# Performance work log

Hardware: AMD Instinct MI355X
Metric: run time of the kernel (lower is better)

The kernel has to match this reference:

```python
import jax, jax.numpy as jnp
import numpy as np

N_QUBITS = 8
N_LAYERS = 2
DIM = 1 << N_QUBITS

# Precompute Pauli-Z eigenvalues per qubit (PennyLane: wire 0 = most significant bit)
_idx = np.arange(DIM)
_bits = ((_idx[None, :] >> (N_QUBITS - 1 - np.arange(N_QUBITS)[:, None])) & 1)  # [n, 2^n]
Z_EIG = jnp.asarray(1.0 - 2.0 * _bits, dtype=jnp.float32)                      # [n, 2^n]
# CZ diagonal signs for adjacent pairs (q, q+1)
CZ_SIGN = jnp.asarray(1.0 - 2.0 * (_bits[:-1] * _bits[1:]), dtype=jnp.float32)  # [n-1, 2^n]


def _rx(t):
    c = jnp.cos(0.5 * t).astype(jnp.complex64)
    s = jnp.sin(0.5 * t).astype(jnp.complex64)
    return jnp.stack([jnp.stack([c, -1j * s], -1), jnp.stack([-1j * s, c], -1)], -2)


def _ry(t):
    c = jnp.cos(0.5 * t).astype(jnp.complex64)
    s = jnp.sin(0.5 * t).astype(jnp.complex64)
    return jnp.stack([jnp.stack([c, -s], -1), jnp.stack([s, c], -1)], -2)


def _rz(t):
    e = jnp.exp(-0.5j * t.astype(jnp.complex64))
    z = jnp.zeros_like(e)
    return jnp.stack([jnp.stack([e, z], -1), jnp.stack([z, jnp.conj(e)], -1)], -2)


def _apply_1q(state, gate, q):
    # state: [B, 2^n]; gate: [B,2,2] (data-dependent angle) or [2,2] (shared weight)
    B = state.shape[0]
    L, R = 1 << q, 1 << (N_QUBITS - q - 1)
    st = state.reshape(B, L, 2, R)
    if gate.ndim == 3:
        st = jnp.einsum('bij,bljr->blir', gate, st)
    else:
        st = jnp.einsum('ij,bljr->blir', gate, st)
    return st.reshape(B, DIM)


def _circuit(angles, q_weights):
    # angles: [B, 3*n] real; q_weights: [n_layers, 2*n]
    B = angles.shape[0]
    state = jnp.zeros((B, DIM), dtype=jnp.complex64).at[:, 0].set(1.0)
    for l in range(N_LAYERS):
        for q in range(N_QUBITS):
            state = _apply_1q(state, _rx(angles[:, 3 * q]), q)
            state = _apply_1q(state, _ry(angles[:, 3 * q + 1]), q)
            state = _apply_1q(state, _rz(angles[:, 3 * q + 2]), q)
        for q in range(N_QUBITS):  # ansatz 1: hardware-efficient RY+RZ
            state = _apply_1q(state, _ry(q_weights[l, q]), q)
            state = _apply_1q(state, _rz(q_weights[l, q + N_QUBITS]), q)
        for q in range(N_QUBITS - 1):  # CZ chain (diagonal)
            state = state * CZ_SIGN[q]
    probs = state.real ** 2 + state.imag ** 2          # [B, 2^n]
    return probs @ Z_EIG.T                              # [B, n] expval PauliZ


def setup_inputs() -> dict:
    key = jax.random.key(0)
    ks = jax.random.split(key, 6)
    B = 8192
    return {
        'x': jax.random.normal(ks[0], (B, 64), dtype=jnp.float32),
        'W_adapter': jax.random.normal(ks[1], (3 * N_QUBITS, 64), dtype=jnp.float32) * 0.1,
        'b_adapter': jax.random.normal(ks[2], (3 * N_QUBITS,), dtype=jnp.float32) * 0.1,
        'q_weights': jax.random.normal(ks[3], (N_LAYERS, 2 * N_QUBITS), dtype=jnp.float32),
        'W_fc': jax.random.normal(ks[4], (1, N_QUBITS), dtype=jnp.float32) * 0.1,
        'b_fc': jax.random.normal(ks[5], (1,), dtype=jnp.float32) * 0.1,
    }


def reference(x, W_adapter, b_adapter, q_weights, W_fc, b_fc):
    angles = jnp.arctan(x @ W_adapter.T + b_adapter)   # [B, 3n]
    expvals = _circuit(angles, q_weights)              # [B, n]
    return expvals @ W_fc.T + b_fc                     # [B, 1]
```

## Files before the change

kernel.cpp:

```cpp
#include <hip/hip_runtime.h>
#include <math.h>

#define NQ 8
#define NL 2

template <int CTRL, int RM, int BM>
__device__ __forceinline__ float dpp_add(float v) {
    int o = __builtin_amdgcn_update_dpp(0, __float_as_int(v), CTRL, RM, BM, true);
    return v + __int_as_float(o);
}

__device__ __forceinline__ float wave_total(float v) {
    v = dpp_add<0xB1, 0xF, 0xF>(v);
    v = dpp_add<0x4E, 0xF, 0xF>(v);
    v = dpp_add<0x114, 0xF, 0xE>(v);
    v = dpp_add<0x118, 0xF, 0xC>(v);
    v = dpp_add<0x142, 0xA, 0xF>(v);
    v = dpp_add<0x143, 0xC, 0xF>(v);
    return __int_as_float(__builtin_amdgcn_readlane(__float_as_int(v), 63));
}

__device__ __forceinline__ float read_lane(float v, int l) {
    return __int_as_float(__builtin_amdgcn_readlane(__float_as_int(v), l));
}

template <int P>
__device__ __forceinline__ float partner(float v) {
    int vi = __float_as_int(v);
    if constexpr (P == 0) {
        return __int_as_float(__builtin_amdgcn_update_dpp(vi, vi, 0xB1, 0xF, 0xF, false));
    } else if constexpr (P == 1) {
        return __int_as_float(__builtin_amdgcn_update_dpp(vi, vi, 0x4E, 0xF, 0xF, false));
    } else if constexpr (P == 2) {
        int a = __builtin_amdgcn_update_dpp(vi, vi, 0x104, 0xF, 0x5, false);
        a = __builtin_amdgcn_update_dpp(a, vi, 0x114, 0xF, 0xA, false);
        return __int_as_float(a);
    } else if constexpr (P == 3) {
        int a = __builtin_amdgcn_update_dpp(vi, vi, 0x108, 0xF, 0x3, false);
        a = __builtin_amdgcn_update_dpp(a, vi, 0x118, 0xF, 0xC, false);
        return __int_as_float(a);
    } else if constexpr (P == 4) {
        return __shfl_xor(v, 16, 64);
    } else {
        return __shfl_xor(v, 32, 64);
    }
}

struct SU2 { float ar, ai, br, bi; };

__device__ __forceinline__ void pair_gate(float& r0, float& i0, float& r1, float& i1,
                                          const SU2 g) {
    float nr0 = g.ar * r0 - g.ai * i0 - g.br * r1 - g.bi * i1;
    float ni0 = g.ar * i0 + g.ai * r0 + g.bi * r1 - g.br * i1;
    float nr1 = g.br * r0 - g.bi * i0 + g.ar * r1 + g.ai * i1;
    float ni1 = g.br * i0 + g.bi * r0 + g.ar * i1 - g.ai * r1;
    r0 = nr0; i0 = ni0; r1 = nr1; i1 = ni1;
}

template <int P>
__device__ __forceinline__ void apply_gate(int lane, float (&r)[4], float (&i)[4],
                                           const SU2 g) {
    if constexpr (P == 7) {
        pair_gate(r[0], i[0], r[2], i[2], g);
        pair_gate(r[1], i[1], r[3], i[3], g);
    } else if constexpr (P == 6) {
        pair_gate(r[0], i[0], r[1], i[1], g);
        pair_gate(r[2], i[2], r[3], i[3], g);
    } else {
        float sg = ((lane >> P) & 1) ? 1.0f : -1.0f;
        float Ai = -sg * g.ai;
        float Br =  sg * g.br;
#pragma unroll
        for (int t = 0; t < 4; ++t) {
            float pr = partner<P>(r[t]);
            float pi = partner<P>(i[t]);
            float nr = g.ar * r[t] - Ai * i[t] + Br * pr - g.bi * pi;
            float ni = g.ar * i[t] + Ai * r[t] + Br * pi + g.bi * pr;
            r[t] = nr; i[t] = ni;
        }
    }
}

template <bool LAST>
__device__ __forceinline__ SU2 compose(float ca, float sa, float cb, float sb,
                                       float zc, float zs, float cd, float sd,
                                       float wc, float ws) {
    float pr = cb * ca, pi = sb * sa;
    float qr = sb * ca, qi = -cb * sa;
    float a1r = zc * pr + zs * pi, a1i = zc * pi - zs * pr;
    float b1r = zc * qr - zs * qi, b1i = zc * qi + zs * qr;
    float a2r = cd * a1r - sd * b1r, a2i = cd * a1i - sd * b1i;
    float b2r = sd * a1r + cd * b1r, b2i = sd * a1i + cd * b1i;
    if constexpr (LAST) {
        return {a2r, a2i, b2r, b2i};
    } else {
        float a3r = wc * a2r + ws * a2i, a3i = wc * a2i - ws * a2r;
        float b3r = wc * b2r - ws * b2i, b3i = wc * b2i + ws * b2r;
        return {a3r, a3i, b3r, b3i};
    }
}

template <int L, int Q>
__device__ __forceinline__ void do_qubit(int lane, float (&r)[4], float (&i)[4],
                                         const float (&cc)[24], const float (&sc)[24],
                                         float vc, float vs) {
    constexpr int P = NQ - 1 - Q;
    constexpr bool LAST = (L == NL - 1);
    float cd = read_lane(vc, 16 * L + Q);
    float sd = read_lane(vs, 16 * L + Q);
    float wc = 1.0f, ws = 0.0f;
    if constexpr (!LAST) {
        wc = read_lane(vc, 16 * L + Q + 8);
        ws = read_lane(vs, 16 * L + Q + 8);
    }
    SU2 g = compose<LAST>(cc[3 * Q], sc[3 * Q], cc[3 * Q + 1], sc[3 * Q + 1],
                          cc[3 * Q + 2], sc[3 * Q + 2], cd, sd, wc, ws);
    apply_gate<P>(lane, r, i, g);
}

__global__ __launch_bounds__(256) void qcritic_kernel(
    const float* __restrict__ x,
    const float* __restrict__ Wad,
    const float* __restrict__ bad,
    const float* __restrict__ qw,
    const float* __restrict__ Wfc,
    const float* __restrict__ bfc,
    float* __restrict__ out,
    int B) {
    int tid  = threadIdx.x;
    int lane = tid & 63;
    int b    = blockIdx.x * 4 + (tid >> 6);
    if (b >= B) return;

    float qv = qw[lane & 31];
    float vs_, vc_;
    sincosf(0.5f * qv, &vs_, &vc_);

    float xv = x[b * 64 + lane];
    float cc[24], sc[24];
#pragma unroll
    for (int j = 0; j < 24; ++j) {
        float u  = wave_total(xv * Wad[j * 64 + lane]) + bad[j];
        float ct = rsqrtf(1.0f + u * u);
        float ch = sqrtf(0.5f * (1.0f + ct));
        cc[j] = ch;
        sc[j] = 0.5f * u * ct / ch;
    }

    float r[4] = {0.f, 0.f, 0.f, 0.f};
    float im[4] = {0.f, 0.f, 0.f, 0.f};
    if (lane == 0) r[0] = 1.0f;

    float czs[4];
#pragma unroll
    for (int t = 0; t < 4; ++t) {
        int idx = t * 64 + lane;
        czs[t] = (__popc(idx & (idx >> 1)) & 1) ? -1.0f : 1.0f;
    }

    do_qubit<0, 0>(lane, r, im, cc, sc, vc_, vs_);
    do_qubit<0, 1>(lane, r, im, cc, sc, vc_, vs_);
    do_qubit<0, 2>(lane, r, im, cc, sc, vc_, vs_);
    do_qubit<0, 3>(lane, r, im, cc, sc, vc_, vs_);
    do_qubit<0, 4>(lane, r, im, cc, sc, vc_, vs_);
    do_qubit<0, 5>(lane, r, im, cc, sc, vc_, vs_);
    do_qubit<0, 6>(lane, r, im, cc, sc, vc_, vs_);
    do_qubit<0, 7>(lane, r, im, cc, sc, vc_, vs_);
#pragma unroll
    for (int t = 0; t < 4; ++t) { r[t] *= czs[t]; im[t] *= czs[t]; }

    do_qubit<1, 0>(lane, r, im, cc, sc, vc_, vs_);
    do_qubit<1, 1>(lane, r, im, cc, sc, vc_, vs_);
    do_qubit<1, 2>(lane, r, im, cc, sc, vc_, vs_);
    do_qubit<1, 3>(lane, r, im, cc, sc, vc_, vs_);
    do_qubit<1, 4>(lane, r, im, cc, sc, vc_, vs_);
    do_qubit<1, 5>(lane, r, im, cc, sc, vc_, vs_);
    do_qubit<1, 6>(lane, r, im, cc, sc, vc_, vs_);
    do_qubit<1, 7>(lane, r, im, cc, sc, vc_, vs_);

    float glow = 0.0f;
#pragma unroll
    for (int k = 2; k < 8; ++k)
        glow += Wfc[k] * (((lane >> (7 - k)) & 1) ? -1.0f : 1.0f);
    float w0 = Wfc[0], w1 = Wfc[1];
    float acc = 0.0f;
#pragma unroll
    for (int t = 0; t < 4; ++t) {
        float g = glow + ((t >> 1) ? -w0 : w0) + ((t & 1) ? -w1 : w1);
        acc += (r[t] * r[t] + im[t] * im[t]) * g;
    }
    float tot = wave_total(acc);
    if (lane == 0) out[b] = tot + bfc[0];
}

extern "C" void kernel_launch(void* const* d_in, const int* in_sizes, int n_in,
                              void* d_out, int out_size, void* d_ws, size_t ws_size,
                              hipStream_t stream) {
    const float* x   = (const float*)d_in[0];
    const float* Wad = (const float*)d_in[1];
    const float* bad = (const float*)d_in[2];
    const float* qw  = (const float*)d_in[3];
    const float* Wfc = (const float*)d_in[4];
    const float* bfc = (const float*)d_in[5];
    float* out = (float*)d_out;
    int B = in_sizes[0] / 64;
    int grid = (B + 3) / 4;
    qcritic_kernel<<<grid, 256, 0, stream>>>(x, Wad, bad, qw, Wfc, bfc, out, B);
}
```

Measured before the change: 95.40 us.

## Compute gate matrices lane-parallel and pack amplitudes into float2 vectors

Each lane now composes one of the 16 fused gate matrices (qubit Q, layer L) from its selected angles. The matrices are broadcast with readlane, replacing redundant per-gate composition and trig in every lane. Amplitudes are held as float2 vectors so the compiler can emit packed FP32 math on CDNA. The cost is a select tree to choose angles per lane and extra readlanes per gate.

```diff
diff --git a/kernel.cpp b/kernel.cpp
--- a/kernel.cpp
+++ b/kernel.cpp
@@ -1,8 +1,9 @@
 #include <hip/hip_runtime.h>
 #include <math.h>
 
-#define NQ 8
-#define NL 2
+typedef __attribute__((ext_vector_type(2))) float f32x2;
+
+__device__ __forceinline__ f32x2 sp(float s) { f32x2 v; v.x = s; v.y = s; return v; }
 
 template <int CTRL, int RM, int BM>
 __device__ __forceinline__ float dpp_add(float v) {
@@ -46,76 +47,64 @@
     }
 }
 
-struct SU2 { float ar, ai, br, bi; };
+template <int P>
+__device__ __forceinline__ f32x2 partner2(f32x2 v) {
+    f32x2 r; r.x = partner<P>(v.x); r.y = partner<P>(v.y); return r;
+}
 
 __device__ __forceinline__ void pair_gate(float& r0, float& i0, float& r1, float& i1,
-                                          const SU2 g) {
-    float nr0 = g.ar * r0 - g.ai * i0 - g.br * r1 - g.bi * i1;
-    float ni0 = g.ar * i0 + g.ai * r0 + g.bi * r1 - g.br * i1;
-    float nr1 = g.br * r0 - g.bi * i0 + g.ar * r1 + g.ai * i1;
-    float ni1 = g.br * i0 + g.bi * r0 + g.ar * i1 - g.ai * r1;
+                                          float ar, float ai, float br, float bi) {
+    float nr0 = ar * r0 - ai * i0 - br * r1 - bi * i1;
+    float ni0 = ar * i0 + ai * r0 + bi * r1 - br * i1;
+    float nr1 = br * r0 - bi * i0 + ar * r1 + ai * i1;
+    float ni1 = br * i0 + bi * r0 + ar * i1 - ai * r1;
     r0 = nr0; i0 = ni0; r1 = nr1; i1 = ni1;
 }
 
+__device__ __forceinline__ void pair_gate2(f32x2& r0, f32x2& i0, f32x2& r1, f32x2& i1,
+                                           float ar, float ai, float br, float bi) {
+    f32x2 va = sp(ar), vi = sp(ai), vb = sp(br), vc = sp(bi);
+    f32x2 nr0 = va * r0 - vi * i0 - vb * r1 - vc * i1;
+    f32x2 ni0 = va * i0 + vi * r0 + vc * r1 - vb * i1;
+    f32x2 nr1 = vb * r0 - vc * i0 + va * r1 + vi * i1;
+    f32x2 ni1 = vb * i0 + vc * r0 + va * i1 - vi * r1;
+    r0 = nr0; i0 = ni0; r1 = nr1; i1 = ni1;
+}
+
 template <int P>
-__device__ __forceinline__ void apply_gate(int lane, float (&r)[4], float (&i)[4],
-                                           const SU2 g) {
+__device__ __forceinline__ void cross_gate(int lane, f32x2& Ar, f32x2& Ai, f32x2& Br, f32x2& Bi,
+                                           float gar, float gai, float gbr, float gbi) {
+    float sg = ((lane >> P) & 1) ? 1.0f : -1.0f;
+    f32x2 vAr = sp(gar), vAi = sp(-sg * gai), vBr = sp(sg * gbr), vBi = sp(gbi);
+    f32x2 pr = partner2<P>(Ar), pi = partner2<P>(Ai);
+    f32x2 nAr = vAr * Ar - vAi * Ai + vBr * pr - vBi * pi;
+    f32x2 nAi = vAr * Ai + vAi * Ar + vBr * pi + vBi * pr;
+    Ar = nAr; Ai = nAi;
+    pr = partner2<P>(Br); pi = partner2<P>(Bi);
+    f32x2 nBr = vAr * Br - vAi * Bi + vBr * pr - vBi * pi;
+    f32x2 nBi = vAr * Bi + vAi * Br + vBr * pi + vBi * pr;
+    Br = nBr; Bi = nBi;
+}
+
+template <int G>
+__device__ __forceinline__ void apply_g(int lane, f32x2& Ar, f32x2& Ai, f32x2& Br, f32x2& Bi,
+                                        float garv, float gaiv, float gbrv, float gbiv) {
+    constexpr int Q = G & 7;
+    constexpr int P = 7 - Q;
+    float ar = read_lane(garv, G), ai = read_lane(gaiv, G);
+    float br = read_lane(gbrv, G), bi = read_lane(gbiv, G);
     if constexpr (P == 7) {
-        pair_gate(r[0], i[0], r[2], i[2], g);
-        pair_gate(r[1], i[1], r[3], i[3], g);
+        pair_gate2(Ar, Ai, Br, Bi, ar, ai, br, bi);
     } else if constexpr (P == 6) {
-        pair_gate(r[0], i[0], r[1], i[1], g);
-        pair_gate(r[2], i[2], r[3], i[3], g);
+        float r0 = Ar.x, i0 = Ai.x, r1 = Ar.y, i1 = Ai.y;
+        pair_gate(r0, i0, r1, i1, ar, ai, br, bi);
+        Ar.x = r0; Ai.x = i0; Ar.y = r1; Ai.y = i1;
+        r0 = Br.x; i0 = Bi.x; r1 = Br.y; i1 = Bi.y;
+        pair_gate(r0, i0, r1, i1, ar, ai, br, bi);
+        Br.x = r0; Bi.x = i0; Br.y = r1; Bi.y = i1;
     } else {
-        float sg = ((lane >> P) & 1) ? 1.0f : -1.0f;
-        float Ai = -sg * g.ai;
-        float Br =  sg * g.br;
-#pragma unroll
-        for (int t = 0; t < 4; ++t) {
-            float pr = partner<P>(r[t]);
-            float pi = partner<P>(i[t]);
-            float nr = g.ar * r[t] - Ai * i[t] + Br * pr - g.bi * pi;
-            float ni = g.ar * i[t] + Ai * r[t] + Br * pi + g.bi * pr;
-            r[t] = nr; i[t] = ni;
-        }
-    }
-}
-
-template <bool LAST>
-__device__ __forceinline__ SU2 compose(float ca, float sa, float cb, float sb,
-                                       float zc, float zs, float cd, float sd,
-                                       float wc, float ws) {
-    float pr = cb * ca, pi = sb * sa;
-    float qr = sb * ca, qi = -cb * sa;
-    float a1r = zc * pr + zs * pi, a1i = zc * pi - zs * pr;
-    float b1r = zc * qr - zs * qi, b1i = zc * qi + zs * qr;
-    float a2r = cd * a1r - sd * b1r, a2i = cd * a1i - sd * b1i;
-    float b2r = sd * a1r + cd * b1r, b2i = sd * a1i + cd * b1i;
-    if constexpr (LAST) {
-        return {a2r, a2i, b2r, b2i};
-    } else {
-        float a3r = wc * a2r + ws * a2i, a3i = wc * a2i - ws * a2r;
-        float b3r = wc * b2r - ws * b2i, b3i = wc * b2i + ws * b2r;
-        return {a3r, a3i, b3r, b3i};
-    }
-}
-
-template <int L, int Q>
-__device__ __forceinline__ void do_qubit(int lane, float (&r)[4], float (&i)[4],
-                                         const float (&cc)[24], const float (&sc)[24],
-                                         float vc, float vs) {
-    constexpr int P = NQ - 1 - Q;
-    constexpr bool LAST = (L == NL - 1);
-    float cd = read_lane(vc, 16 * L + Q);
-    float sd = read_lane(vs, 16 * L + Q);
-    float wc = 1.0f, ws = 0.0f;
-    if constexpr (!LAST) {
-        wc = read_lane(vc, 16 * L + Q + 8);
-        ws = read_lane(vs, 16 * L + Q + 8);
-    }
-    SU2 g = compose<LAST>(cc[3 * Q], sc[3 * Q], cc[3 * Q + 1], sc[3 * Q + 1],
-                          cc[3 * Q + 2], sc[3 * Q + 2], cd, sd, wc, ws);
-    apply_gate<P>(lane, r, i, g);
+        cross_gate<P>(lane, Ar, Ai, Br, Bi, ar, ai, br, bi);
+    }
 }
 
 __global__ __launch_bounds__(256) void qcritic_kernel(
@@ -127,69 +116,95 @@
     const float* __restrict__ bfc,
     float* __restrict__ out,
     int B) {
-    int tid  = threadIdx.x;
+    int tid = threadIdx.x;
     int lane = tid & 63;
-    int b    = blockIdx.x * 4 + (tid >> 6);
+    int b = blockIdx.x * 4 + (tid >> 6);
     if (b >= B) return;
 
-    float qv = qw[lane & 31];
-    float vs_, vc_;
-    sincosf(0.5f * qv, &vs_, &vc_);
-
     float xv = x[b * 64 + lane];
-    float cc[24], sc[24];
-#pragma unroll
-    for (int j = 0; j < 24; ++j) {
-        float u  = wave_total(xv * Wad[j * 64 + lane]) + bad[j];
-        float ct = rsqrtf(1.0f + u * u);
-        float ch = sqrtf(0.5f * (1.0f + ct));
-        cc[j] = ch;
-        sc[j] = 0.5f * u * ct / ch;
-    }
-
-    float r[4] = {0.f, 0.f, 0.f, 0.f};
-    float im[4] = {0.f, 0.f, 0.f, 0.f};
-    if (lane == 0) r[0] = 1.0f;
-
-    float czs[4];
-#pragma unroll
-    for (int t = 0; t < 4; ++t) {
-        int idx = t * 64 + lane;
-        czs[t] = (__popc(idx & (idx >> 1)) & 1) ? -1.0f : 1.0f;
-    }
-
-    do_qubit<0, 0>(lane, r, im, cc, sc, vc_, vs_);
-    do_qubit<0, 1>(lane, r, im, cc, sc, vc_, vs_);
-    do_qubit<0, 2>(lane, r, im, cc, sc, vc_, vs_);
-    do_qubit<0, 3>(lane, r, im, cc, sc, vc_, vs_);
-    do_qubit<0, 4>(lane, r, im, cc, sc, vc_, vs_);
-    do_qubit<0, 5>(lane, r, im, cc, sc, vc_, vs_);
-    do_qubit<0, 6>(lane, r, im, cc, sc, vc_, vs_);
-    do_qubit<0, 7>(lane, r, im, cc, sc, vc_, vs_);
-#pragma unroll
-    for (int t = 0; t < 4; ++t) { r[t] *= czs[t]; im[t] *= czs[t]; }
-
-    do_qubit<1, 0>(lane, r, im, cc, sc, vc_, vs_);
-    do_qubit<1, 1>(lane, r, im, cc, sc, vc_, vs_);
-    do_qubit<1, 2>(lane, r, im, cc, sc, vc_, vs_);
-    do_qubit<1, 3>(lane, r, im, cc, sc, vc_, vs_);
-    do_qubit<1, 4>(lane, r, im, cc, sc, vc_, vs_);
-    do_qubit<1, 5>(lane, r, im, cc, sc, vc_, vs_);
-    do_qubit<1, 6>(lane, r, im, cc, sc, vc_, vs_);
-    do_qubit<1, 7>(lane, r, im, cc, sc, vc_, vs_);
+    float u[24];
+#pragma unroll
+    for (int j = 0; j < 24; ++j)
+        u[j] = wave_total(xv * Wad[j * 64 + lane]) + bad[j];
+
+    int Q = lane & 7;
+    int L = (lane >> 3) & 1;
+    bool b0 = Q & 1, b1 = Q & 2, b2 = Q & 4;
+    float uq[3];
+#pragma unroll
+    for (int k = 0; k < 3; ++k) {
+        float m01 = b0 ? u[3 + k] : u[0 + k];
+        float m23 = b0 ? u[9 + k] : u[6 + k];
+        float m45 = b0 ? u[15 + k] : u[12 + k];
+        float m67 = b0 ? u[21 + k] : u[18 + k];
+        float m03 = b1 ? m23 : m01;
+        float m47 = b1 ? m67 : m45;
+        uq[k] = b2 ? m47 : m03;
+    }
+    float ch[3], sh[3];
+#pragma unroll
+    for (int k = 0; k < 3; ++k) {
+        float v = uq[k];
+        float ct = rsqrtf(1.0f + v * v);
+        ch[k] = sqrtf(0.5f * (1.0f + ct));
+        sh[k] = __fdividef(0.5f * v * ct, ch[k]);
+    }
+    float cd, sd, wc, ws;
+    __sincosf(0.5f * qw[(L << 4) + Q], &sd, &cd);
+    __sincosf(0.5f * qw[(L << 4) + Q + 8], &ws, &wc);
+    if (L == 1) { wc = 1.0f; ws = 0.0f; }
+    float ca = ch[0], sa = sh[0], cb = ch[1], sb = sh[1], zc = ch[2], zs = sh[2];
+    float pr = cb * ca, pi = sb * sa;
+    float qr = sb * ca, qi = -cb * sa;
+    float a1r = zc * pr + zs * pi, a1i = zc * pi - zs * pr;
+    float b1r = zc * qr - zs * qi, b1i = zc * qi + zs * qr;
+    float a2r = cd * a1r - sd * b1r, a2i = cd * a1i - sd * b1i;
+    float b2r = sd * a1r + cd * b1r, b2i = sd * a1i + cd * b1i;
+    float garv = wc * a2r + ws * a2i, gaiv = wc * a2i - ws * a2r;
+    float gbrv = wc * b2r - ws * b2i, gbiv = wc * b2i + ws * b2r;
+
+    f32x2 Ar, Ai, Br, Bi;
+    Ar.x = (lane == 0) ? 1.0f : 0.0f; Ar.y = 0.0f;
+    Ai = sp(0.0f); Br = sp(0.0f); Bi = sp(0.0f);
+
+    f32x2 czA, czB;
+    {
+        int i0 = lane, i1 = 64 + lane, i2 = 128 + lane, i3 = 192 + lane;
+        czA.x = (__popc(i0 & (i0 >> 1)) & 1) ? -1.0f : 1.0f;
+        czA.y = (__popc(i1 & (i1 >> 1)) & 1) ? -1.0f : 1.0f;
+        czB.x = (__popc(i2 & (i2 >> 1)) & 1) ? -1.0f : 1.0f;
+        czB.y = (__popc(i3 & (i3 >> 1)) & 1) ? -1.0f : 1.0f;
+    }
+
+    apply_g<0>(lane, Ar, Ai, Br, Bi, garv, gaiv, gbrv, gbiv);
+    apply_g<1>(lane, Ar, Ai, Br, Bi, garv, gaiv, gbrv, gbiv);
+    apply_g<2>(lane, Ar, Ai, Br, Bi, garv, gaiv, gbrv, gbiv);
+    apply_g<3>(lane, Ar, Ai, Br, Bi, garv, gaiv, gbrv, gbiv);
+    apply_g<4>(lane, Ar, Ai, Br, Bi, garv, gaiv, gbrv, gbiv);
+    apply_g<5>(lane, Ar, Ai, Br, Bi, garv, gaiv, gbrv, gbiv);
+    apply_g<6>(lane, Ar, Ai, Br, Bi, garv, gaiv, gbrv, gbiv);
+    apply_g<7>(lane, Ar, Ai, Br, Bi, garv, gaiv, gbrv, gbiv);
+    Ar *= czA; Ai *= czA; Br *= czB; Bi *= czB;
+
+    apply_g<8>(lane, Ar, Ai, Br, Bi, garv, gaiv, gbrv, gbiv);
+    apply_g<9>(lane, Ar, Ai, Br, Bi, garv, gaiv, gbrv, gbiv);
+    apply_g<10>(lane, Ar, Ai, Br, Bi, garv, gaiv, gbrv, gbiv);
+    apply_g<11>(lane, Ar, Ai, Br, Bi, garv, gaiv, gbrv, gbiv);
+    apply_g<12>(lane, Ar, Ai, Br, Bi, garv, gaiv, gbrv, gbiv);
+    apply_g<13>(lane, Ar, Ai, Br, Bi, garv, gaiv, gbrv, gbiv);
+    apply_g<14>(lane, Ar, Ai, Br, Bi, garv, gaiv, gbrv, gbiv);
+    apply_g<15>(lane, Ar, Ai, Br, Bi, garv, gaiv, gbrv, gbiv);
 
     float glow = 0.0f;
 #pragma unroll
     for (int k = 2; k < 8; ++k)
         glow += Wfc[k] * (((lane >> (7 - k)) & 1) ? -1.0f : 1.0f);
     float w0 = Wfc[0], w1 = Wfc[1];
-    float acc = 0.0f;
-#pragma unroll
-    for (int t = 0; t < 4; ++t) {
-        float g = glow + ((t >> 1) ? -w0 : w0) + ((t & 1) ? -w1 : w1);
-        acc += (r[t] * r[t] + im[t] * im[t]) * g;
-    }
-    float tot = wave_total(acc);
+    f32x2 gA, gB;
+    gA.x = glow + w0 + w1; gA.y = glow + w0 - w1;
+    gB.x = glow - w0 + w1; gB.y = glow - w0 - w1;
+    f32x2 acc2 = (Ar * Ar + Ai * Ai) * gA + (Br * Br + Bi * Bi) * gB;
+    float tot = wave_total(acc2.x + acc2.y);
     if (lane == 0) out[b] = tot + bfc[0];
 }
 
```

Result: faster. 80.22 us (-15.9%).
